# Optimization experiments

Hardware: AMD Instinct MI355X
Metric: run time of the kernel (lower is better)

The kernel has to match this reference:

```python
import jax, jax.numpy as jnp
import numpy as np

# Module config (init_kwargs): nodes = (64, 64)
NX, NY_NODES = 64, 64


def setup_inputs() -> dict:
    key = jax.random.key(0)
    data = jax.random.normal(key, (4, 3, 1024, 1024), dtype=jnp.float32)
    return {"data": data}


def reference(data):
    B, C, H, W = data.shape
    scale = W // NX                    # = 16
    ny = H // scale                    # grid rows (= 64 here)
    nx = NX
    N = nx * ny                        # num_nodes = 4096
    p = scale - 1                      # original slices x1:x2 with x2=x1+scale-1 -> (scale-1) pixels

    # [B, C, ny, p, nx, p] top-left (scale-1)x(scale-1) sub-patch of each grid cell
    patches = data.reshape(B, C, ny, scale, nx, scale)[:, :, :, :p, :, :p]

    # L1 affinity between vertically / horizontally adjacent patches
    dv = jnp.abs(patches[:, :, 1:] - patches[:, :, :-1]).sum(axis=(1, 3, 5))          # [B, ny-1, nx]
    dh = jnp.abs(patches[:, :, :, :, 1:] - patches[:, :, :, :, :-1]).sum(axis=(1, 3, 5))  # [B, ny, nx-1]

    node = jnp.arange(ny)[:, None] * nx + jnp.arange(nx)[None, :]  # node_id = x + y*nx

    A = jnp.zeros((B, N, N), dtype=data.dtype)
    # vertical edges: self<->up/down
    lo_v = node[1:, :].ravel()   # lower cell of each vertical pair
    hi_v = node[:-1, :].ravel()  # upper cell
    dv_f = dv.reshape(B, -1)
    A = A.at[:, lo_v, hi_v].set(dv_f)   # self -> up
    A = A.at[:, hi_v, lo_v].set(dv_f)   # self -> down
    # horizontal edges: self<->left/right
    le_h = node[:, :-1].ravel()
    ri_h = node[:, 1:].ravel()
    dh_f = dh.reshape(B, -1)
    A = A.at[:, le_h, ri_h].set(dh_f)   # self -> right
    A = A.at[:, ri_h, le_h].set(dh_f)   # self -> left

    return A, data
```

## Files before the change

kernel.cpp:

```cpp
#include <hip/hip_runtime.h>

#define BB 4
#define CC 3
#define HH 1024
#define WW 1024
#define NXG 64
#define NYG 64
#define SCALE 16
#define PP 15
#define NNODE 4096

static const long long A_ELEMS    = (long long)BB * NNODE * NNODE;
static const long long DATA_ELEMS = (long long)BB * CC * HH * WW;

#define NV_PER_B 4032
#define NH_PER_B 4032
#define NV_TOT   16128
#define NE_TOT   32256

#define K1_COPY_BLOCKS 512
#define K1_EDGE_BLOCKS 8064

__global__ __launch_bounds__(256) void edge_copy_kernel(const float* __restrict__ data,
                                                        float* __restrict__ ws,
                                                        float* __restrict__ out) {
    if (blockIdx.x < K1_COPY_BLOCKS) {
        long long i = (long long)blockIdx.x * 256 + threadIdx.x;
        const long long stride = (long long)K1_COPY_BLOCKS * 256;
        const float4* __restrict__ src = (const float4*)data;
        float4* __restrict__ dst = (float4*)(out + A_ELEMS);
        const long long nvec = DATA_ELEMS / 4;
        for (; i < nvec; i += stride) dst[i] = src[i];
        return;
    }
    const int wave = (blockIdx.x - K1_COPY_BLOCKS) * 4 + (threadIdx.x >> 6);
    const int lane = threadIdx.x & 63;
    const int r = lane >> 2;
    const int q = lane & 3;

    int b, y, x;
    long long delta;
    if (wave < NV_TOT) {
        const int e = wave;
        b = e / NV_PER_B; const int rem = e - b * NV_PER_B;
        y = rem >> 6; x = rem & 63;
        delta = (long long)SCALE * WW;
    } else {
        const int e = wave - NV_TOT;
        b = e / NH_PER_B; const int rem = e - b * NH_PER_B;
        y = rem / 63; x = rem - y * 63;
        delta = SCALE;
    }

    const float* p0 = data + (((long long)(b * CC)) * HH + (long long)y * SCALE + r) * WW
                           + x * SCALE + q * 4;
    float s = 0.f;
    if (r < PP) {
        #pragma unroll
        for (int c = 0; c < CC; ++c) {
            const float* p = p0 + (long long)c * HH * WW;
            const float4 a  = *(const float4*)p;
            const float4 nb = *(const float4*)(p + delta);
            float d = fabsf(nb.x - a.x) + fabsf(nb.y - a.y) + fabsf(nb.z - a.z);
            if (q != 3) d += fabsf(nb.w - a.w);
            s += d;
        }
    }
    #pragma unroll
    for (int off = 32; off; off >>= 1) s += __shfl_down(s, off, 64);
    if (lane == 0) ws[wave] = s;
}

__global__ __launch_bounds__(256) void row_kernel(const float* __restrict__ ws,
                                                  float* __restrict__ out) {
    const int wid  = blockIdx.x * 4 + (threadIdx.x >> 6);
    const int lane = threadIdx.x & 63;
    const int b = wid >> 12;
    const int n = wid & (NNODE - 1);
    const int y = n >> 6, x = n & 63;

    const bool hasUp = y > 0, hasDown = y < NYG - 1;
    const bool hasLeft = x > 0, hasRight = x < NXG - 1;

    float vUp = 0.f, vDown = 0.f, vLeft = 0.f, vRight = 0.f;
    if (hasUp)    vUp    = ws[b * NV_PER_B + (y - 1) * 64 + x];
    if (hasDown)  vDown  = ws[b * NV_PER_B + y * 64 + x];
    if (hasLeft)  vLeft  = ws[NV_TOT + b * NH_PER_B + y * 63 + (x - 1)];
    if (hasRight) vRight = ws[NV_TOT + b * NH_PER_B + y * 63 + x];

    const int kUp    = __builtin_amdgcn_readfirstlane(hasUp    ? ((n - 64) >> 8) : -1);
    const int kDown  = __builtin_amdgcn_readfirstlane(hasDown  ? ((n + 64) >> 8) : -1);
    const int kLeft  = __builtin_amdgcn_readfirstlane(hasLeft  ? ((n - 1)  >> 8) : -1);
    const int kRight = __builtin_amdgcn_readfirstlane(hasRight ? ((n + 1)  >> 8) : -1);
    const int lUp    = __builtin_amdgcn_readfirstlane(((n - 64) >> 2) & 63);
    const int lDown  = __builtin_amdgcn_readfirstlane(((n + 64) >> 2) & 63);
    const int lLeft  = __builtin_amdgcn_readfirstlane(((n - 1)  >> 2) & 63);
    const int lRight = __builtin_amdgcn_readfirstlane(((n + 1)  >> 2) & 63);

    const int compUD = n & 3;
    const int compL  = (n - 1) & 3;
    const int compR  = (n + 1) & 3;

    float4 pUp, pDown, pLeft, pRight;
    pUp.x    = compUD == 0 ? vUp : 0.f;    pUp.y    = compUD == 1 ? vUp : 0.f;
    pUp.z    = compUD == 2 ? vUp : 0.f;    pUp.w    = compUD == 3 ? vUp : 0.f;
    pDown.x  = compUD == 0 ? vDown : 0.f;  pDown.y  = compUD == 1 ? vDown : 0.f;
    pDown.z  = compUD == 2 ? vDown : 0.f;  pDown.w  = compUD == 3 ? vDown : 0.f;
    pLeft.x  = compL == 0 ? vLeft : 0.f;   pLeft.y  = compL == 1 ? vLeft : 0.f;
    pLeft.z  = compL == 2 ? vLeft : 0.f;   pLeft.w  = compL == 3 ? vLeft : 0.f;
    pRight.x = compR == 0 ? vRight : 0.f;  pRight.y = compR == 1 ? vRight : 0.f;
    pRight.z = compR == 2 ? vRight : 0.f;  pRight.w = compR == 3 ? vRight : 0.f;

    float4* rowp = (float4*)(out + ((long long)b * NNODE + n) * NNODE);
    #pragma unroll
    for (int k = 0; k < 16; ++k) {
        float4 v = make_float4(0.f, 0.f, 0.f, 0.f);
        if (k == kUp)    { if (lane == lUp)    { v.x += pUp.x;    v.y += pUp.y;    v.z += pUp.z;    v.w += pUp.w;    } }
        if (k == kDown)  { if (lane == lDown)  { v.x += pDown.x;  v.y += pDown.y;  v.z += pDown.z;  v.w += pDown.w;  } }
        if (k == kLeft)  { if (lane == lLeft)  { v.x += pLeft.x;  v.y += pLeft.y;  v.z += pLeft.z;  v.w += pLeft.w;  } }
        if (k == kRight) { if (lane == lRight) { v.x += pRight.x; v.y += pRight.y; v.z += pRight.z; v.w += pRight.w; } }
        rowp[k * 64 + lane] = v;
    }
}

extern "C" void kernel_launch(void* const* d_in, const int* in_sizes, int n_in,
                              void* d_out, int out_size, void* d_ws, size_t ws_size,
                              hipStream_t stream) {
    const float* data = (const float*)d_in[0];
    float* out = (float*)d_out;
    float* ws  = (float*)d_ws;

    edge_copy_kernel<<<K1_COPY_BLOCKS + K1_EDGE_BLOCKS, 256, 0, stream>>>(data, ws, out);
    row_kernel<<<4096, 256, 0, stream>>>(ws, out);
}
```

Before: 360.1 us.

## Replace row-writing kernel with memset plus direct edge scatter

Drops the second kernel that built every dense adjacency row from a workspace of edge sums. The output matrix is now zeroed with hipMemsetAsync, and each edge wave writes its two symmetric entries straight into it. This removes the workspace round trip and the per-row select logic. The memset still writes the full 256MB matrix, so the saving depends on whether the driver fill is faster than the custom row kernel, and the scattered stores are uncoalesced.

```diff
diff --git a/kernel.cpp b/kernel.cpp
--- a/kernel.cpp
+++ b/kernel.cpp
@@ -18,38 +18,40 @@
 #define NV_TOT   16128
 #define NE_TOT   32256
 
-#define K1_COPY_BLOCKS 512
-#define K1_EDGE_BLOCKS 8064
+#define COPY_BLOCKS 512
+#define EDGE_BLOCKS 8064
 
-__global__ __launch_bounds__(256) void edge_copy_kernel(const float* __restrict__ data,
-                                                        float* __restrict__ ws,
-                                                        float* __restrict__ out) {
-    if (blockIdx.x < K1_COPY_BLOCKS) {
+__global__ __launch_bounds__(256) void edge_copy_scatter(const float* __restrict__ data,
+                                                         float* __restrict__ out) {
+    if (blockIdx.x < COPY_BLOCKS) {
         long long i = (long long)blockIdx.x * 256 + threadIdx.x;
-        const long long stride = (long long)K1_COPY_BLOCKS * 256;
+        const long long stride = (long long)COPY_BLOCKS * 256;
         const float4* __restrict__ src = (const float4*)data;
         float4* __restrict__ dst = (float4*)(out + A_ELEMS);
         const long long nvec = DATA_ELEMS / 4;
         for (; i < nvec; i += stride) dst[i] = src[i];
         return;
     }
-    const int wave = (blockIdx.x - K1_COPY_BLOCKS) * 4 + (threadIdx.x >> 6);
+
+    const int wave = (blockIdx.x - COPY_BLOCKS) * 4 + (threadIdx.x >> 6);
     const int lane = threadIdx.x & 63;
     const int r = lane >> 2;
     const int q = lane & 3;
 
-    int b, y, x;
+    int b, y, x, n_lo, n_hi;
     long long delta;
     if (wave < NV_TOT) {
         const int e = wave;
         b = e / NV_PER_B; const int rem = e - b * NV_PER_B;
         y = rem >> 6; x = rem & 63;
         delta = (long long)SCALE * WW;
+        n_lo = y * NXG + x; n_hi = n_lo + NXG;
     } else {
         const int e = wave - NV_TOT;
         b = e / NH_PER_B; const int rem = e - b * NH_PER_B;
         y = rem / 63; x = rem - y * 63;
         delta = SCALE;
+        n_lo = y * NXG + x; n_hi = n_lo + 1;
     }
 
     const float* p0 = data + (((long long)(b * CC)) * HH + (long long)y * SCALE + r) * WW
@@ -68,58 +70,11 @@
     }
     #pragma unroll
     for (int off = 32; off; off >>= 1) s += __shfl_down(s, off, 64);
-    if (lane == 0) ws[wave] = s;
-}
 
-__global__ __launch_bounds__(256) void row_kernel(const float* __restrict__ ws,
-                                                  float* __restrict__ out) {
-    const int wid  = blockIdx.x * 4 + (threadIdx.x >> 6);
-    const int lane = threadIdx.x & 63;
-    const int b = wid >> 12;
-    const int n = wid & (NNODE - 1);
-    const int y = n >> 6, x = n & 63;
-
-    const bool hasUp = y > 0, hasDown = y < NYG - 1;
-    const bool hasLeft = x > 0, hasRight = x < NXG - 1;
-
-    float vUp = 0.f, vDown = 0.f, vLeft = 0.f, vRight = 0.f;
-    if (hasUp)    vUp    = ws[b * NV_PER_B + (y - 1) * 64 + x];
-    if (hasDown)  vDown  = ws[b * NV_PER_B + y * 64 + x];
-    if (hasLeft)  vLeft  = ws[NV_TOT + b * NH_PER_B + y * 63 + (x - 1)];
-    if (hasRight) vRight = ws[NV_TOT + b * NH_PER_B + y * 63 + x];
-
-    const int kUp    = __builtin_amdgcn_readfirstlane(hasUp    ? ((n - 64) >> 8) : -1);
-    const int kDown  = __builtin_amdgcn_readfirstlane(hasDown  ? ((n + 64) >> 8) : -1);
-    const int kLeft  = __builtin_amdgcn_readfirstlane(hasLeft  ? ((n - 1)  >> 8) : -1);
-    const int kRight = __builtin_amdgcn_readfirstlane(hasRight ? ((n + 1)  >> 8) : -1);
-    const int lUp    = __builtin_amdgcn_readfirstlane(((n - 64) >> 2) & 63);
-    const int lDown  = __builtin_amdgcn_readfirstlane(((n + 64) >> 2) & 63);
-    const int lLeft  = __builtin_amdgcn_readfirstlane(((n - 1)  >> 2) & 63);
-    const int lRight = __builtin_amdgcn_readfirstlane(((n + 1)  >> 2) & 63);
-
-    const int compUD = n & 3;
-    const int compL  = (n - 1) & 3;
-    const int compR  = (n + 1) & 3;
-
-    float4 pUp, pDown, pLeft, pRight;
-    pUp.x    = compUD == 0 ? vUp : 0.f;    pUp.y    = compUD == 1 ? vUp : 0.f;
-    pUp.z    = compUD == 2 ? vUp : 0.f;    pUp.w    = compUD == 3 ? vUp : 0.f;
-    pDown.x  = compUD == 0 ? vDown : 0.f;  pDown.y  = compUD == 1 ? vDown : 0.f;
-    pDown.z  = compUD == 2 ? vDown : 0.f;  pDown.w  = compUD == 3 ? vDown : 0.f;
-    pLeft.x  = compL == 0 ? vLeft : 0.f;   pLeft.y  = compL == 1 ? vLeft : 0.f;
-    pLeft.z  = compL == 2 ? vLeft : 0.f;   pLeft.w  = compL == 3 ? vLeft : 0.f;
-    pRight.x = compR == 0 ? vRight : 0.f;  pRight.y = compR == 1 ? vRight : 0.f;
-    pRight.z = compR == 2 ? vRight : 0.f;  pRight.w = compR == 3 ? vRight : 0.f;
-
-    float4* rowp = (float4*)(out + ((long long)b * NNODE + n) * NNODE);
-    #pragma unroll
-    for (int k = 0; k < 16; ++k) {
-        float4 v = make_float4(0.f, 0.f, 0.f, 0.f);
-        if (k == kUp)    { if (lane == lUp)    { v.x += pUp.x;    v.y += pUp.y;    v.z += pUp.z;    v.w += pUp.w;    } }
-        if (k == kDown)  { if (lane == lDown)  { v.x += pDown.x;  v.y += pDown.y;  v.z += pDown.z;  v.w += pDown.w;  } }
-        if (k == kLeft)  { if (lane == lLeft)  { v.x += pLeft.x;  v.y += pLeft.y;  v.z += pLeft.z;  v.w += pLeft.w;  } }
-        if (k == kRight) { if (lane == lRight) { v.x += pRight.x; v.y += pRight.y; v.z += pRight.z; v.w += pRight.w; } }
-        rowp[k * 64 + lane] = v;
+    if (lane == 0) {
+        float* Ab = out + (long long)b * NNODE * NNODE;
+        Ab[(long long)n_hi * NNODE + n_lo] = s;
+        Ab[(long long)n_lo * NNODE + n_hi] = s;
     }
 }
 
@@ -128,8 +83,8 @@
                               hipStream_t stream) {
     const float* data = (const float*)d_in[0];
     float* out = (float*)d_out;
-    float* ws  = (float*)d_ws;
 
-    edge_copy_kernel<<<K1_COPY_BLOCKS + K1_EDGE_BLOCKS, 256, 0, stream>>>(data, ws, out);
-    row_kernel<<<4096, 256, 0, stream>>>(ws, out);
+    hipMemsetAsync(out, 0, (size_t)A_ELEMS * sizeof(float), stream);
+
+    edge_copy_scatter<<<COPY_BLOCKS + EDGE_BLOCKS, 256, 0, stream>>>(data, out);
 }
```

Result: no change. 355.6 us (-1.3%).
